# Performance work log

Measured on AMD Instinct MI355X. Metric: run time of the kernel, lower is better.

The kernel has to match this reference:

```python
import jax, jax.numpy as jnp
import numpy as np

B, N, D, K = 8, 2048, 3, 16
CIN, CD, COUT = 64, 16, 128
C = CIN + CD            # 80, channels after concat
DM = 2                  # depth_multiplier = ceil(128/80)
EPS = 1e-5


def _bn(x, g, b):
    # BatchNorm1d in training mode: biased batch stats over axis 0
    m = x.mean(0)
    v = x.var(0)
    return (x - m) * jax.lax.rsqrt(v + EPS) * g + b


def setup_inputs() -> dict:
    key = jax.random.key(0)
    ks = jax.random.split(key, 12)
    f = lambda k, shp: (jax.random.normal(k, shp, jnp.float32) * 0.05)
    return dict(
        x=jax.random.normal(ks[0], (B, N, CIN), jnp.float32),
        pos=jax.random.normal(ks[1], (B, N, D), jnp.float32),
        # mlp1: Linear(D,CD) ELU BN, Linear(CD,CD) ELU BN
        W1=f(ks[2], (D, CD)), b1=jnp.zeros((CD,)), g1=jnp.ones((CD,)), be1=jnp.zeros((CD,)),
        W2=f(ks[3], (CD, CD)), b2=jnp.zeros((CD,)), g2=jnp.ones((CD,)), be2=jnp.zeros((CD,)),
        # mlp2: Linear(D*K,K^2) ELU BN, grouped Conv1d(K,K^2,K) ELU BN, grouped Conv1d BN
        Wl=f(ks[4], (D * K, K * K)), bl=jnp.zeros((K * K,)), gl=jnp.ones((K * K,)), bel=jnp.zeros((K * K,)),
        WcA=f(ks[5], (K, K, K)), bcA=jnp.zeros((K, K)), gA=jnp.ones((K * K,)), beA=jnp.zeros((K * K,)),
        WcB=f(ks[6], (K, K, K)), bcB=jnp.zeros((K, K)), gB=jnp.ones((K * K,)), beB=jnp.zeros((K * K,)),
        # final depthwise Conv1d(C, C*DM, K, groups=C) + Linear(C*DM, COUT)
        Wd=f(ks[7], (C, DM, K)), bd=jnp.zeros((C, DM)),
        Wo=f(ks[8], (C * DM, COUT)), bo=jnp.zeros((COUT,)),
    )


def reference(x, pos, W1, b1, g1, be1, W2, b2, g2, be2,
              Wl, bl, gl, bel, WcA, bcA, gA, beA, WcB, bcB, gB, beB,
              Wd, bd, Wo, bo):
    # --- KNN via squared pairwise distances (same ordering as torch.cdist) ---
    sq = jnp.sum(pos * pos, -1)                                     # (B,N)
    d2 = sq[:, :, None] + sq[:, None, :] - 2.0 * jnp.einsum('bnd,bmd->bnm', pos, pos)
    _, idx = jax.lax.top_k(-d2, K)                                  # (B,N,K) nearest (incl. self)
    gather = jax.vmap(lambda a, i: a[i])                            # batched fancy-gather
    pos_j = gather(pos, idx)                                        # (B,N,K,D)
    d = pos[:, :, None, :] - pos_j                                  # relative coords (B,N,K,D)

    # --- mlp1 over B*N*K points -> lifted features x_star ---
    h = d.reshape(-1, D)                                            # (BNK,D)
    h = _bn(jax.nn.elu(h @ W1 + b1), g1, be1)
    h = _bn(jax.nn.elu(h @ W2 + b2), g2, be2)                       # (BNK,CD)

    xj = gather(x, idx)                                             # (B,N,K,CIN)
    xs = jnp.concatenate([h.reshape(B, N, K, CD), xj], -1)          # (B,N,K,C)
    xs = xs.reshape(B * N, K, C).transpose(0, 2, 1)                 # (BN,C,K)

    # --- mlp2: learned KxK transform from relative coords ---
    t = d.reshape(B * N, K * D)
    t = _bn(jax.nn.elu(t @ Wl + bl), gl, bel).reshape(-1, K, K)
    # grouped Conv1d(K, K^2, K, groups=K): out[b,g,o] = sum_k t[b,g,k]*W[g,o,k] + bias[g,o]
    t = jax.nn.elu(jnp.einsum('bgk,gok->bgo', t, WcA) + bcA)
    t = _bn(t.reshape(-1, K * K), gA, beA).reshape(-1, K, K)
    t = jnp.einsum('bgk,gok->bgo', t, WcB) + bcB
    t = _bn(t.reshape(-1, K * K), gB, beB).reshape(-1, K, K)        # (BN,K,K)

    # --- apply transform, depthwise conv, final linear ---
    xt = jnp.einsum('bck,bko->bco', xs, t)                          # (BN,C,K)
    o = jnp.einsum('bck,cmk->bcm', xt, Wd) + bd                     # (BN,C,DM)
    o = o.reshape(B * N, C * DM) @ Wo + bo                          # (BN,COUT)
    return o.reshape(B, N, COUT)
```

## Files before the change

kernel.cpp:

```cpp
#include <hip/hip_runtime.h>
#include <math.h>

#define NN 2048
#define KNbr 16
#define BNpts 16384
#define BNKr  262144

__device__ __forceinline__ float eluf(float v) { return v > 0.f ? v : expm1f(v); }

__global__ __launch_bounds__(256) void knn_kernel(const float* __restrict__ pos,
                                                  int* __restrict__ idxout,
                                                  float* __restrict__ drel) {
  int wav = threadIdx.x >> 6, lane = threadIdx.x & 63;
  int bn = blockIdx.x*4 + wav;
  int b = bn >> 11, n = bn & (NN - 1);
  const float* pb = pos + (size_t)b * NN * 3;
  float qx = pb[n*3], qy = pb[n*3+1], qz = pb[n*3+2];
  float sqn = __fadd_rn(__fadd_rn(__fmul_rn(qx,qx), __fmul_rn(qy,qy)), __fmul_rn(qz,qz));
  double kreg[32];
#pragma unroll
  for (int s = 0; s < 32; ++s) {
    int m = s*64 + lane;
    float px = pb[m*3], py = pb[m*3+1], pz = pb[m*3+2];
    float sqm = __fadd_rn(__fadd_rn(__fmul_rn(px,px), __fmul_rn(py,py)), __fmul_rn(pz,pz));
    float dot = __fmaf_rn(qz, pz, __fmaf_rn(qy, py, __fmul_rn(qx, px)));
    float d2  = __fsub_rn(__fadd_rn(sqn, sqm), __fmul_rn(2.0f, dot));
    unsigned int bits = __float_as_uint(d2);
    unsigned int uf = bits ^ (((unsigned int)((int)bits >> 31)) >> 1);
    kreg[s] = __hiloint2double((int)uf, m);
  }
  const double KINF = __hiloint2double(0x7FF00000, 0);
  for (int k = 0; k < KNbr; ++k) {
    double g0 = fmin(fmin(kreg[0],  kreg[1]),  fmin(kreg[2],  kreg[3]));
    double g1 = fmin(fmin(kreg[4],  kreg[5]),  fmin(kreg[6],  kreg[7]));
    double g2 = fmin(fmin(kreg[8],  kreg[9]),  fmin(kreg[10], kreg[11]));
    double g3 = fmin(fmin(kreg[12], kreg[13]), fmin(kreg[14], kreg[15]));
    double g4 = fmin(fmin(kreg[16], kreg[17]), fmin(kreg[18], kreg[19]));
    double g5 = fmin(fmin(kreg[20], kreg[21]), fmin(kreg[22], kreg[23]));
    double g6 = fmin(fmin(kreg[24], kreg[25]), fmin(kreg[26], kreg[27]));
    double g7 = fmin(fmin(kreg[28], kreg[29]), fmin(kreg[30], kreg[31]));
    double bk = fmin(fmin(fmin(g0, g1), fmin(g2, g3)),
                     fmin(fmin(g4, g5), fmin(g6, g7)));
#pragma unroll
    for (int off = 32; off > 0; off >>= 1) {
      double ok = __shfl_xor(bk, off);
      bk = fmin(bk, ok);
    }
    int fi = __builtin_amdgcn_readfirstlane(__double2loint(bk));
    if (lane == 0) {
      idxout[bn*KNbr + k] = fi;
      drel[(size_t)(bn*KNbr + k)*3 + 0] = __fsub_rn(qx, pb[fi*3+0]);
      drel[(size_t)(bn*KNbr + k)*3 + 1] = __fsub_rn(qy, pb[fi*3+1]);
      drel[(size_t)(bn*KNbr + k)*3 + 2] = __fsub_rn(qz, pb[fi*3+2]);
    }
    bool owner = (lane == (fi & 63));
#define CLR(i) case i: if (owner) kreg[i] = KINF; break;
    switch (fi >> 6) {
      CLR(0)  CLR(1)  CLR(2)  CLR(3)  CLR(4)  CLR(5)  CLR(6)  CLR(7)
      CLR(8)  CLR(9)  CLR(10) CLR(11) CLR(12) CLR(13) CLR(14) CLR(15)
      CLR(16) CLR(17) CLR(18) CLR(19) CLR(20) CLR(21) CLR(22) CLR(23)
      CLR(24) CLR(25) CLR(26) CLR(27) CLR(28) CLR(29) CLR(30) CLR(31)
    }
#undef CLR
  }
}

__global__ __launch_bounds__(256) void s1a_kernel(const float* __restrict__ drel,
                                                  const float* __restrict__ W1,
                                                  const float* __restrict__ b1,
                                                  double* __restrict__ part1) {
  __shared__ float sW[64];
  int tid = threadIdx.x;
  if (tid < 48) sW[tid] = W1[tid];
  if (tid < 16) sW[48+tid] = b1[tid];
  __syncthreads();
  const float4* src4 = (const float4*)(drel + ((size_t)blockIdx.x*1024 + tid*4)*3);
  float a[12];
#pragma unroll
  for (int q = 0; q < 3; ++q) { float4 t = src4[q]; a[q*4]=t.x; a[q*4+1]=t.y; a[q*4+2]=t.z; a[q*4+3]=t.w; }
  float s[16], s2[16];
#pragma unroll
  for (int c = 0; c < 16; ++c) { s[c] = 0.f; s2[c] = 0.f; }
#pragma unroll
  for (int i = 0; i < 4; ++i) {
    float a0 = a[i*3], a1 = a[i*3+1], a2 = a[i*3+2];
#pragma unroll
    for (int c = 0; c < 16; ++c) {
      float v = a0*sW[c] + a1*sW[16+c] + a2*sW[32+c] + sW[48+c];
      float e = eluf(v);
      s[c] += e; s2[c] += e*e;
    }
  }
  __shared__ float wred[4][32];
  int lane = tid & 63, wav = tid >> 6;
#pragma unroll
  for (int j = 0; j < 32; ++j) {
    float v = (j < 16) ? s[j] : s2[j-16];
    for (int sh = 32; sh > 0; sh >>= 1) v += __shfl_down(v, sh);
    if (lane == 0) wred[wav][j] = v;
  }
  __syncthreads();
  if (tid < 32)
    part1[(size_t)blockIdx.x*32 + tid] =
      (double)wred[0][tid] + (double)wred[1][tid] + (double)wred[2][tid] + (double)wred[3][tid];
}

__global__ __launch_bounds__(256) void s1b_kernel(const float* __restrict__ drel,
                                                  const float* __restrict__ W1,
                                                  const float* __restrict__ b1,
                                                  const float* __restrict__ W2,
                                                  const float* __restrict__ b2,
                                                  const double* __restrict__ part1,
                                                  const float* __restrict__ g1,
                                                  const float* __restrict__ be1,
                                                  double* __restrict__ part2) {
  int tid = threadIdx.x;
  __shared__ double red[8][32];
  __shared__ float fsc1[16], fsh1[16];
  __shared__ float sW[64];
  __shared__ float sW2t[256];
  {
    int j = tid & 31, grp = tid >> 5;
    double v = 0.0;
    for (int bk = grp; bk < 256; bk += 8) v += part1[(size_t)bk*32 + j];
    red[grp][j] = v;
  }
  if (tid < 48) sW[tid] = W1[tid];
  if (tid < 16) sW[48+tid] = b1[tid];
  sW2t[tid] = W2[(tid & 15)*16 + (tid >> 4)];
  __syncthreads();
  if (tid < 32) {
    double v = 0.0;
    for (int g = 0; g < 8; ++g) v += red[g][tid];
    red[0][tid] = v;
  }
  __syncthreads();
  if (tid < 16) {
    double S = red[0][tid], S2 = red[0][16 + tid];
    double m = S/262144.0, var = S2/262144.0 - m*m;
    double sc = (double)g1[tid]/sqrt(var + 1e-5);
    fsc1[tid] = (float)sc;
    fsh1[tid] = (float)((double)be1[tid] - m*sc);
  }
  __syncthreads();
  const float4* src4 = (const float4*)(drel + ((size_t)blockIdx.x*1024 + tid*4)*3);
  float a[12];
#pragma unroll
  for (int q = 0; q < 3; ++q) { float4 t = src4[q]; a[q*4]=t.x; a[q*4+1]=t.y; a[q*4+2]=t.z; a[q*4+3]=t.w; }
  float s[16], s2[16];
#pragma unroll
  for (int c = 0; c < 16; ++c) { s[c] = 0.f; s2[c] = 0.f; }
#pragma unroll
  for (int i = 0; i < 4; ++i) {
    float a0 = a[i*3], a1 = a[i*3+1], a2 = a[i*3+2];
    float y[16];
#pragma unroll
    for (int c = 0; c < 16; ++c) {
      float v = a0*sW[c] + a1*sW[16+c] + a2*sW[32+c] + sW[48+c];
      y[c] = eluf(v)*fsc1[c] + fsh1[c];
    }
#pragma unroll
    for (int c2 = 0; c2 < 16; ++c2) {
      float v = b2[c2];
      const float4* w4 = (const float4*)&sW2t[c2*16];
#pragma unroll
      for (int j4 = 0; j4 < 4; ++j4) {
        float4 ww = w4[j4];
        v += y[j4*4]*ww.x + y[j4*4+1]*ww.y + y[j4*4+2]*ww.z + y[j4*4+3]*ww.w;
      }
      float e = eluf(v);
      s[c2] += e; s2[c2] += e*e;
    }
  }
  __shared__ float wred[4][32];
  int lane = tid & 63, wav = tid >> 6;
#pragma unroll
  for (int j = 0; j < 32; ++j) {
    float v = (j < 16) ? s[j] : s2[j-16];
    for (int sh = 32; sh > 0; sh >>= 1) v += __shfl_down(v, sh);
    if (lane == 0) wred[wav][j] = v;
  }
  __syncthreads();
  if (tid < 32)
    part2[(size_t)blockIdx.x*32 + tid] =
      (double)wred[0][tid] + (double)wred[1][tid] + (double)wred[2][tid] + (double)wred[3][tid];
}

__global__ __launch_bounds__(256) void s2l_kernel(const float* __restrict__ drel,
                                                  const float* __restrict__ Wl,
                                                  const float* __restrict__ bl,
                                                  float* __restrict__ tL,
                                                  double* __restrict__ partL) {
  __shared__ float srows[64*48];
  int tid = threadIdx.x;
  const float* src = drel + (size_t)blockIdx.x * 3072;
  for (int i = tid; i < 3072; i += 256) srows[i] = src[i];
  float w[48];
#pragma unroll
  for (int j = 0; j < 48; ++j) w[j] = Wl[j*256 + tid];
  float bias = bl[tid];
  __syncthreads();
  double s = 0.0, s2 = 0.0;
  for (int r = 0; r < 64; ++r) {
    float v = bias;
    const float4* sr = (const float4*)&srows[r*48];
#pragma unroll
    for (int j4 = 0; j4 < 12; ++j4) {
      float4 a4 = sr[j4];
      v += a4.x*w[j4*4] + a4.y*w[j4*4+1] + a4.z*w[j4*4+2] + a4.w*w[j4*4+3];
    }
    float e = eluf(v);
    tL[(size_t)(blockIdx.x*64 + r)*256 + tid] = e;
    double ed = (double)e;
    s += ed; s2 += ed*ed;
  }
  partL[(size_t)blockIdx.x*512 + tid]       = s;
  partL[(size_t)blockIdx.x*512 + 256 + tid] = s2;
}

template<int DO_ELU>
__global__ __launch_bounds__(256) void s2conv_kernel(const double* __restrict__ partIn,
                                                     const float* __restrict__ gIn,
                                                     const float* __restrict__ beIn,
                                                     const float* __restrict__ Wc,
                                                     const float* __restrict__ bc,
                                                     float* __restrict__ tBuf,
                                                     double* __restrict__ partOut) {
  int tid = threadIdx.x;
  double S = 0.0, S2 = 0.0;
  for (int bk = 0; bk < 256; ++bk) {
    S  += partIn[(size_t)bk*512 + tid];
    S2 += partIn[(size_t)bk*512 + 256 + tid];
  }
  double m = S/16384.0, var = S2/16384.0 - m*m;
  double scd = (double)gIn[tid]/sqrt(var + 1e-5);
  float sc = (float)scd, sh = (float)((double)beIn[tid] - m*scd);
  int g = tid >> 4, o = tid & 15;
  float w[16];
#pragma unroll
  for (int k = 0; k < 16; ++k) w[k] = Wc[g*256 + o*16 + k];
  float bias = bc[tid];
  __shared__ float sin_[16*256];
  double s = 0.0, s2 = 0.0;
  float* buf = tBuf + (size_t)blockIdx.x*64*256;
  for (int chunk = 0; chunk < 4; ++chunk) {
    __syncthreads();
    for (int rr = 0; rr < 16; ++rr)
      sin_[rr*256 + tid] = buf[(chunk*16 + rr)*256 + tid]*sc + sh;
    __syncthreads();
    for (int rr = 0; rr < 16; ++rr) {
      float v = bias;
      const float4* row4 = (const float4*)&sin_[rr*256 + g*16];
#pragma unroll
      for (int k4 = 0; k4 < 4; ++k4) {
        float4 a4 = row4[k4];
        v += a4.x*w[k4*4] + a4.y*w[k4*4+1] + a4.z*w[k4*4+2] + a4.w*w[k4*4+3];
      }
      float e = DO_ELU ? eluf(v) : v;
      buf[(chunk*16 + rr)*256 + tid] = e;
      double ed = (double)e;
      s += ed; s2 += ed*ed;
    }
  }
  partOut[(size_t)blockIdx.x*512 + tid]       = s;
  partOut[(size_t)blockIdx.x*512 + 256 + tid] = s2;
}

__global__ void bnall_kernel(const double* __restrict__ part1,
                             const double* __restrict__ part2,
                             const double* __restrict__ partB,
                             const float* __restrict__ g1, const float* __restrict__ be1,
                             const float* __restrict__ g2, const float* __restrict__ be2,
                             const float* __restrict__ gB, const float* __restrict__ beB,
                             float* __restrict__ bnp) {
  int tid = threadIdx.x;
  if (tid < 32) {
    int c = tid & 15;
    const double* P = (tid < 16) ? part1 : part2;
    double S = 0.0, S2 = 0.0;
    for (int bk = 0; bk < 256; ++bk) { S += P[(size_t)bk*32 + c]; S2 += P[(size_t)bk*32 + 16 + c]; }
    double m = S/262144.0, var = S2/262144.0 - m*m;
    const float* g  = (tid < 16) ? g1 : g2;
    const float* be = (tid < 16) ? be1 : be2;
    double sc = (double)g[c]/sqrt(var + 1e-5);
    int off = (tid < 16) ? 0 : 32;
    bnp[off + c]      = (float)sc;
    bnp[off + 16 + c] = (float)((double)be[c] - m*sc);
  }
  {
    double S = 0.0, S2 = 0.0;
    for (int bk = 0; bk < 256; ++bk) { S += partB[(size_t)bk*512 + tid]; S2 += partB[(size_t)bk*512 + 256 + tid]; }
    double m = S/16384.0, var = S2/16384.0 - m*m;
    double sc = (double)gB[tid]/sqrt(var + 1e-5);
    bnp[64 + tid]  = (float)sc;
    bnp[320 + tid] = (float)((double)beB[tid] - m*sc);
  }
}

__global__ __launch_bounds__(256) void final_kernel(const float* __restrict__ x,
                                                    const int* __restrict__ idxbuf,
                                                    const float* __restrict__ drel,
                                                    const float* __restrict__ tB,
                                                    const float* __restrict__ bnp,
                                                    const float* __restrict__ W1,
                                                    const float* __restrict__ b1,
                                                    const float* __restrict__ W2,
                                                    const float* __restrict__ b2,
                                                    const float* __restrict__ Wd,
                                                    const float* __restrict__ bd,
                                                    const float* __restrict__ Wo,
                                                    const float* __restrict__ bo,
                                                    float* __restrict__ out) {
  int tid = threadIdx.x;
  int bn0 = blockIdx.x*2;
  int b = bn0 >> 11;
  __shared__ float sbn1[32], sbn2[32];
  __shared__ float sBs[256], sBh[256];
  __shared__ int   sidx[32];
  __shared__ float sdrel[96];
  __shared__ float sW1[48], sb1[16], sb2[16];
  __shared__ float sW2t[256];
  __shared__ float tmat[512];
  __shared__ float hs[2][16][17];
  __shared__ float xst[2][16][80];
  __shared__ float ovs[2][160];
  if (tid < 32) { sbn1[tid] = bnp[tid]; sbn2[tid] = bnp[32 + tid]; }
  sBs[tid] = bnp[64 + tid];
  sBh[tid] = bnp[320 + tid];
  if (tid < 32) sidx[tid] = idxbuf[bn0*16 + tid];
  if (tid < 96) sdrel[tid] = drel[(size_t)bn0*48 + tid];
  if (tid < 48) sW1[tid] = W1[tid];
  if (tid < 16) { sb1[tid] = b1[tid]; sb2[tid] = b2[tid]; }
  sW2t[tid] = W2[(tid & 15)*16 + (tid >> 4)];
  __syncthreads();
  for (int i = tid; i < 512; i += 256) {
    int c = i & 255;
    tmat[i] = tB[(size_t)bn0*256 + i]*sBs[c] + sBh[c];
  }
  for (int i = tid; i < 512; i += 256) {
    int pt = i >> 8, k = (i >> 4) & 15, c = i & 15;
    float a0 = sdrel[pt*48 + k*3], a1 = sdrel[pt*48 + k*3 + 1], a2 = sdrel[pt*48 + k*3 + 2];
    float v = a0*sW1[c] + a1*sW1[16+c] + a2*sW1[32+c] + sb1[c];
    hs[pt][k][c] = eluf(v)*sbn1[c] + sbn1[16+c];
  }
  __syncthreads();
  for (int i = tid; i < 512; i += 256) {
    int pt = i >> 8, k = (i >> 4) & 15, c2 = i & 15;
    float v = sb2[c2];
    const float4* w4 = (const float4*)&sW2t[c2*16];
    float* hrow = &hs[pt][k][0];
#pragma unroll
    for (int j4 = 0; j4 < 4; ++j4) {
      float4 ww = w4[j4];
      v += hrow[j4*4]*ww.x + hrow[j4*4+1]*ww.y + hrow[j4*4+2]*ww.z + hrow[j4*4+3]*ww.w;
    }
    xst[pt][k][c2] = eluf(v)*sbn2[c2] + sbn2[16+c2];
  }
  for (int i = tid; i < 512; i += 256) {
    int pt = i >> 8, k = (i >> 4) & 15, c4 = i & 15;
    float4 xv = *(const float4*)&x[((size_t)b*NN + sidx[pt*16 + k])*64 + c4*4];
    *(float4*)&xst[pt][k][16 + c4*4] = xv;
  }
  __syncthreads();
  if (tid < 160) {
    int pt = (tid >= 80) ? 1 : 0;
    int c = tid - pt*80;
    float xtr[16];
#pragma unroll
    for (int o = 0; o < 16; ++o) xtr[o] = 0.f;
#pragma unroll
    for (int k = 0; k < 16; ++k) {
      float xv = xst[pt][k][c];
      const float* tm = &tmat[pt*256 + k*16];
#pragma unroll
      for (int o = 0; o < 16; ++o) xtr[o] += xv*tm[o];
    }
    float v0 = bd[c*2], v1 = bd[c*2 + 1];
#pragma unroll
    for (int k = 0; k < 16; ++k) {
      v0 += xtr[k]*Wd[c*32 + k];
      v1 += xtr[k]*Wd[c*32 + 16 + k];
    }
    ovs[pt][c*2]     = v0;
    ovs[pt][c*2 + 1] = v1;
  }
  __syncthreads();
  {
    int pt0 = tid >> 7, co = tid & 127;
    float v = bo[co];
    for (int i = 0; i < 160; ++i) v += ovs[pt0][i]*Wo[i*128 + co];
    out[(size_t)(bn0 + pt0)*128 + co] = v;
  }
}

extern "C" void kernel_launch(void* const* d_in, const int* in_sizes, int n_in,
                              void* d_out, int out_size, void* d_ws, size_t ws_size,
                              hipStream_t stream) {
  (void)in_sizes; (void)n_in; (void)out_size; (void)ws_size;
  const float* x   = (const float*)d_in[0];
  const float* pos = (const float*)d_in[1];
  const float* W1  = (const float*)d_in[2];
  const float* b1  = (const float*)d_in[3];
  const float* g1  = (const float*)d_in[4];
  const float* be1 = (const float*)d_in[5];
  const float* W2  = (const float*)d_in[6];
  const float* b2  = (const float*)d_in[7];
  const float* g2  = (const float*)d_in[8];
  const float* be2 = (const float*)d_in[9];
  const float* Wl  = (const float*)d_in[10];
  const float* bl  = (const float*)d_in[11];
  const float* gl  = (const float*)d_in[12];
  const float* bel = (const float*)d_in[13];
  const float* WcA = (const float*)d_in[14];
  const float* bcA = (const float*)d_in[15];
  const float* gA  = (const float*)d_in[16];
  const float* beA = (const float*)d_in[17];
  const float* WcB = (const float*)d_in[18];
  const float* bcB = (const float*)d_in[19];
  const float* gB  = (const float*)d_in[20];
  const float* beB = (const float*)d_in[21];
  const float* Wd  = (const float*)d_in[22];
  const float* bd  = (const float*)d_in[23];
  const float* Wo  = (const float*)d_in[24];
  const float* bo  = (const float*)d_in[25];
  float* out = (float*)d_out;

  char* ws = (char*)d_ws;
  int*    idxbuf = (int*)ws;
  float*  drel   = (float*)(ws + (1u<<20));
  float*  bufX   = (float*)(ws + (4u<<20));
  double* part1  = (double*)(ws + (20u<<20));
  double* part2  = (double*)(ws + (20u<<20) + (64u<<10));
  double* partL  = (double*)(ws + (20u<<20) + (128u<<10));
  double* partA  = (double*)(ws + (20u<<20) + (128u<<10) + (1u<<20));
  double* partB  = (double*)(ws + (20u<<20) + (128u<<10) + (2u<<20));
  float*  bnp    = (float*)(ws + (20u<<20) + (128u<<10) + (3u<<20));

  knn_kernel<<<dim3(4096), dim3(256), 0, stream>>>(pos, idxbuf, drel);
  s1a_kernel<<<dim3(256), dim3(256), 0, stream>>>(drel, W1, b1, part1);
  s1b_kernel<<<dim3(256), dim3(256), 0, stream>>>(drel, W1, b1, W2, b2, part1, g1, be1, part2);
  s2l_kernel<<<dim3(256), dim3(256), 0, stream>>>(drel, Wl, bl, bufX, partL);
  s2conv_kernel<1><<<dim3(256), dim3(256), 0, stream>>>(partL, gl, bel, WcA, bcA, bufX, partA);
  s2conv_kernel<0><<<dim3(256), dim3(256), 0, stream>>>(partA, gA, beA, WcB, bcB, bufX, partB);
  bnall_kernel<<<dim3(1), dim3(256), 0, stream>>>(part1, part2, partB, g1, be1, g2, be2, gB, beB, bnp);
  final_kernel<<<dim3(8192), dim3(256), 0, stream>>>(x, idxbuf, drel, bufX, bnp,
                                                     W1, b1, W2, b2, Wd, bd, Wo, bo, out);
}
```

Baseline: 337.4 us.

## Hoist BN stat reduction into separate kernel and process four points per final block

Each of the 256 s2conv blocks previously re-reduced all 256 blocks of partial BN sums. A single-block reduction kernel now computes scale and shift once, and s2conv only reads them, at the cost of two extra kernel launches. The final kernel now handles four points per block instead of two, so each thread computes two points and each weight load of Wd and Wo is reused twice. This halves the grid but raises shared memory and register use.

```diff
diff --git a/kernel.cpp b/kernel.cpp
--- a/kernel.cpp
+++ b/kernel.cpp
@@ -218,23 +218,36 @@
   partL[(size_t)blockIdx.x*512 + 256 + tid] = s2;
 }
 
+__global__ __launch_bounds__(1024) void bnred_kernel(const double* __restrict__ part,
+                                                     const float* __restrict__ g,
+                                                     const float* __restrict__ be,
+                                                     float* __restrict__ bnp) {
+  __shared__ double red[1024];
+  int t = threadIdx.x;
+  int c = t & 255, half = (t >> 8) & 1, q = t >> 9;
+  const double* p = part + (size_t)(q*128)*512 + half*256 + c;
+  double v = 0.0;
+  for (int bk = 0; bk < 128; ++bk) v += p[(size_t)bk*512];
+  red[t] = v;
+  __syncthreads();
+  if (t < 256) {
+    double S  = red[t]       + red[512 + t];
+    double S2 = red[256 + t] + red[768 + t];
+    double m = S/16384.0, var = S2/16384.0 - m*m;
+    double sc = (double)g[t]/sqrt(var + 1e-5);
+    bnp[t]       = (float)sc;
+    bnp[256 + t] = (float)((double)be[t] - m*sc);
+  }
+}
+
 template<int DO_ELU>
-__global__ __launch_bounds__(256) void s2conv_kernel(const double* __restrict__ partIn,
-                                                     const float* __restrict__ gIn,
-                                                     const float* __restrict__ beIn,
+__global__ __launch_bounds__(256) void s2conv_kernel(const float* __restrict__ bnIn,
                                                      const float* __restrict__ Wc,
                                                      const float* __restrict__ bc,
                                                      float* __restrict__ tBuf,
                                                      double* __restrict__ partOut) {
   int tid = threadIdx.x;
-  double S = 0.0, S2 = 0.0;
-  for (int bk = 0; bk < 256; ++bk) {
-    S  += partIn[(size_t)bk*512 + tid];
-    S2 += partIn[(size_t)bk*512 + 256 + tid];
-  }
-  double m = S/16384.0, var = S2/16384.0 - m*m;
-  double scd = (double)gIn[tid]/sqrt(var + 1e-5);
-  float sc = (float)scd, sh = (float)((double)beIn[tid] - m*scd);
+  float sc = bnIn[tid], sh = bnIn[256 + tid];
   int g = tid >> 4, o = tid & 15;
   float w[16];
 #pragma unroll
@@ -312,39 +325,39 @@
                                                     const float* __restrict__ bo,
                                                     float* __restrict__ out) {
   int tid = threadIdx.x;
-  int bn0 = blockIdx.x*2;
+  int bn0 = blockIdx.x*4;
   int b = bn0 >> 11;
   __shared__ float sbn1[32], sbn2[32];
   __shared__ float sBs[256], sBh[256];
-  __shared__ int   sidx[32];
-  __shared__ float sdrel[96];
+  __shared__ int   sidx[64];
+  __shared__ float sdrel[192];
   __shared__ float sW1[48], sb1[16], sb2[16];
   __shared__ float sW2t[256];
-  __shared__ float tmat[512];
-  __shared__ float hs[2][16][17];
-  __shared__ float xst[2][16][80];
-  __shared__ float ovs[2][160];
+  __shared__ float tmat[1024];
+  __shared__ float hs[4][16][17];
+  __shared__ float xst[4][16][80];
+  __shared__ float ovs[4][160];
   if (tid < 32) { sbn1[tid] = bnp[tid]; sbn2[tid] = bnp[32 + tid]; }
   sBs[tid] = bnp[64 + tid];
   sBh[tid] = bnp[320 + tid];
-  if (tid < 32) sidx[tid] = idxbuf[bn0*16 + tid];
-  if (tid < 96) sdrel[tid] = drel[(size_t)bn0*48 + tid];
+  if (tid < 64) sidx[tid] = idxbuf[bn0*16 + tid];
+  if (tid < 192) sdrel[tid] = drel[(size_t)bn0*48 + tid];
   if (tid < 48) sW1[tid] = W1[tid];
   if (tid < 16) { sb1[tid] = b1[tid]; sb2[tid] = b2[tid]; }
   sW2t[tid] = W2[(tid & 15)*16 + (tid >> 4)];
   __syncthreads();
-  for (int i = tid; i < 512; i += 256) {
+  for (int i = tid; i < 1024; i += 256) {
     int c = i & 255;
     tmat[i] = tB[(size_t)bn0*256 + i]*sBs[c] + sBh[c];
   }
-  for (int i = tid; i < 512; i += 256) {
+  for (int i = tid; i < 1024; i += 256) {
     int pt = i >> 8, k = (i >> 4) & 15, c = i & 15;
     float a0 = sdrel[pt*48 + k*3], a1 = sdrel[pt*48 + k*3 + 1], a2 = sdrel[pt*48 + k*3 + 2];
     float v = a0*sW1[c] + a1*sW1[16+c] + a2*sW1[32+c] + sb1[c];
     hs[pt][k][c] = eluf(v)*sbn1[c] + sbn1[16+c];
   }
   __syncthreads();
-  for (int i = tid; i < 512; i += 256) {
+  for (int i = tid; i < 1024; i += 256) {
     int pt = i >> 8, k = (i >> 4) & 15, c2 = i & 15;
     float v = sb2[c2];
     const float4* w4 = (const float4*)&sW2t[c2*16];
@@ -356,7 +369,7 @@
     }
     xst[pt][k][c2] = eluf(v)*sbn2[c2] + sbn2[16+c2];
   }
-  for (int i = tid; i < 512; i += 256) {
+  for (int i = tid; i < 1024; i += 256) {
     int pt = i >> 8, k = (i >> 4) & 15, c4 = i & 15;
     float4 xv = *(const float4*)&x[((size_t)b*NN + sidx[pt*16 + k])*64 + c4*4];
     *(float4*)&xst[pt][k][16 + c4*4] = xv;
@@ -365,31 +378,46 @@
   if (tid < 160) {
     int pt = (tid >= 80) ? 1 : 0;
     int c = tid - pt*80;
-    float xtr[16];
-#pragma unroll
-    for (int o = 0; o < 16; ++o) xtr[o] = 0.f;
+    float xtr0[16], xtr1[16];
+#pragma unroll
+    for (int o = 0; o < 16; ++o) { xtr0[o] = 0.f; xtr1[o] = 0.f; }
 #pragma unroll
     for (int k = 0; k < 16; ++k) {
-      float xv = xst[pt][k][c];
-      const float* tm = &tmat[pt*256 + k*16];
-#pragma unroll
-      for (int o = 0; o < 16; ++o) xtr[o] += xv*tm[o];
-    }
-    float v0 = bd[c*2], v1 = bd[c*2 + 1];
+      float xv0 = xst[pt][k][c];
+      float xv1 = xst[pt + 2][k][c];
+      const float* tm0 = &tmat[pt*256 + k*16];
+      const float* tm1 = &tmat[(pt + 2)*256 + k*16];
+#pragma unroll
+      for (int o = 0; o < 16; ++o) {
+        xtr0[o] += xv0*tm0[o];
+        xtr1[o] += xv1*tm1[o];
+      }
+    }
+    float b0 = bd[c*2], b1v = bd[c*2 + 1];
+    float v00 = b0, v01 = b1v, v10 = b0, v11 = b1v;
 #pragma unroll
     for (int k = 0; k < 16; ++k) {
-      v0 += xtr[k]*Wd[c*32 + k];
-      v1 += xtr[k]*Wd[c*32 + 16 + k];
-    }
-    ovs[pt][c*2]     = v0;
-    ovs[pt][c*2 + 1] = v1;
+      float w0 = Wd[c*32 + k], w1 = Wd[c*32 + 16 + k];
+      v00 += xtr0[k]*w0; v01 += xtr0[k]*w1;
+      v10 += xtr1[k]*w0; v11 += xtr1[k]*w1;
+    }
+    ovs[pt][c*2]       = v00;
+    ovs[pt][c*2 + 1]   = v01;
+    ovs[pt+2][c*2]     = v10;
+    ovs[pt+2][c*2 + 1] = v11;
   }
   __syncthreads();
   {
     int pt0 = tid >> 7, co = tid & 127;
-    float v = bo[co];
-    for (int i = 0; i < 160; ++i) v += ovs[pt0][i]*Wo[i*128 + co];
-    out[(size_t)(bn0 + pt0)*128 + co] = v;
+    float v0 = bo[co], v1 = v0;
+#pragma unroll 8
+    for (int i = 0; i < 160; ++i) {
+      float wv = Wo[i*128 + co];
+      v0 += ovs[pt0][i]*wv;
+      v1 += ovs[pt0 + 2][i]*wv;
+    }
+    out[(size_t)(bn0 + pt0)*128 + co]     = v0;
+    out[(size_t)(bn0 + pt0 + 2)*128 + co] = v1;
   }
 }
 
@@ -435,14 +463,18 @@
   double* partA  = (double*)(ws + (20u<<20) + (128u<<10) + (1u<<20));
   double* partB  = (double*)(ws + (20u<<20) + (128u<<10) + (2u<<20));
   float*  bnp    = (float*)(ws + (20u<<20) + (128u<<10) + (3u<<20));
+  float*  bnpL   = (float*)(ws + (20u<<20) + (128u<<10) + (3u<<20) + 4096);
+  float*  bnpA   = (float*)(ws + (20u<<20) + (128u<<10) + (3u<<20) + 8192);
 
   knn_kernel<<<dim3(4096), dim3(256), 0, stream>>>(pos, idxbuf, drel);
   s1a_kernel<<<dim3(256), dim3(256), 0, stream>>>(drel, W1, b1, part1);
   s1b_kernel<<<dim3(256), dim3(256), 0, stream>>>(drel, W1, b1, W2, b2, part1, g1, be1, part2);
   s2l_kernel<<<dim3(256), dim3(256), 0, stream>>>(drel, Wl, bl, bufX, partL);
-  s2conv_kernel<1><<<dim3(256), dim3(256), 0, stream>>>(partL, gl, bel, WcA, bcA, bufX, partA);
-  s2conv_kernel<0><<<dim3(256), dim3(256), 0, stream>>>(partA, gA, beA, WcB, bcB, bufX, partB);
+  bnred_kernel<<<dim3(1), dim3(1024), 0, stream>>>(partL, gl, bel, bnpL);
+  s2conv_kernel<1><<<dim3(256), dim3(256), 0, stream>>>(bnpL, WcA, bcA, bufX, partA);
+  bnred_kernel<<<dim3(1), dim3(1024), 0, stream>>>(partA, gA, beA, bnpA);
+  s2conv_kernel<0><<<dim3(256), dim3(256), 0, stream>>>(bnpA, WcB, bcB, bufX, partB);
   bnall_kernel<<<dim3(1), dim3(256), 0, stream>>>(part1, part2, partB, g1, be1, g2, be2, gB, beB, bnp);
-  final_kernel<<<dim3(8192), dim3(256), 0, stream>>>(x, idxbuf, drel, bufX, bnp,
+  final_kernel<<<dim3(4096), dim3(256), 0, stream>>>(x, idxbuf, drel, bufX, bnp,
                                                      W1, b1, W2, b2, Wd, bd, Wo, bo, out);
 }
```

New measurement: 325.1 us, median of 2. 3.6% less time.
